# Optimization experiments

Measured on AMD Instinct MI355X. Metric: run time of the kernel, lower is better.

## Reference

```python
import jax, jax.numpy as jnp
import numpy as np

NHEAD = 4
LAYER_TYPES = ["self", "cross", "self", "cross", "semantic_subspace_cross"]


def _ln(x):
    m = jnp.mean(x, axis=-1, keepdims=True)
    v = jnp.var(x, axis=-1, keepdims=True)
    return (x - m) / jnp.sqrt(v + 1e-5)


def _attn(x, source, q_mask, kv_mask, qW, kW, vW, mW, w1, w2):
    # Faithful GeometryAttentionLayer forward (pe=None, sinusoidal branch).
    bs, L, C = x.shape
    dim = C // NHEAD
    qw = (x @ qW).reshape(bs, L, NHEAD, dim)
    kw = (source @ kW).reshape(bs, -1, NHEAD, dim)
    vw = (source @ vW).reshape(bs, -1, NHEAD, dim)
    a = jnp.einsum('nlhd,nshd->nlsh', qw, kw)
    if q_mask is not None:
        bad = q_mask[:, :, None, None] & (~kv_mask)[:, None, :, None]
        a = jnp.where(bad, -jnp.inf, a)
    a = jax.nn.softmax(a / jnp.sqrt(jnp.asarray(dim, x.dtype)), axis=2)
    o = jnp.einsum('nlsh,nshd->nlhd', a, vw).reshape(bs, L, C)
    msg = _ln(o @ mW)
    h = jnp.concatenate([x, msg], axis=-1)
    msg = _ln(jnp.maximum(h @ w1, 0.0) @ w2)
    return x + msg


def setup_inputs() -> dict:
    key = jax.random.key(0)
    ks = jax.random.split(key, 24)
    B, N, C, D2 = 2, 2048, 256, 384
    G, Lp, nL = 16, 512, len(LAYER_TYPES)
    inp = {
        'src_feat': jax.random.normal(ks[0], (B, N, C), jnp.float32),
        'tgt_feat': jax.random.normal(ks[1], (B, N, C), jnp.float32),
        's_pcd': jax.random.normal(ks[2], (B, N, 3), jnp.float32),
        't_pcd': jax.random.normal(ks[3], (B, N, 3), jnp.float32),
        'src_mask': jnp.ones((B, N), bool),
        'tgt_mask': jnp.ones((B, N), bool),
        'src_sub_ind_padded': jax.random.randint(ks[4], (G, Lp), 0, N + 1),
        'tgt_sub_ind_padded': jax.random.randint(ks[5], (G, Lp), 0, N + 1),
        'src_sub_ind_padded_mask': jnp.ones((G, Lp), bool),
        'tgt_sub_ind_padded_mask': jnp.ones((G, Lp), bool),
        'semantic_masks_valid': jnp.ones((G,), bool),
        'src_2dfeat': jax.random.normal(ks[6], (B, N, D2), jnp.float32),
        'tgt_2dfeat': jax.random.normal(ks[7], (B, N, D2), jnp.float32),
        'data': 0,
        'dinoW': jax.random.normal(ks[8], (D2, C), jnp.float32) / np.sqrt(D2),
        'qW': jax.random.normal(ks[9], (nL, C, C), jnp.float32) / np.sqrt(C),
        'kW': jax.random.normal(ks[10], (nL, C, C), jnp.float32) / np.sqrt(C),
        'vW': jax.random.normal(ks[11], (nL, C, C), jnp.float32) / np.sqrt(C),
        'mW': jax.random.normal(ks[12], (nL, C, C), jnp.float32) / np.sqrt(C),
        'w1': jax.random.normal(ks[13], (nL, 2 * C, 2 * C), jnp.float32) / np.sqrt(2 * C),
        'w2': jax.random.normal(ks[14], (nL, 2 * C, C), jnp.float32) / np.sqrt(2 * C),
    }
    return inp


def reference(src_feat, tgt_feat, s_pcd, t_pcd, src_mask, tgt_mask,
              src_sub_ind_padded, tgt_sub_ind_padded,
              src_sub_ind_padded_mask, tgt_sub_ind_padded_mask,
              semantic_masks_valid, src_2dfeat, tgt_2dfeat, data,
              dinoW, qW, kW, vW, mW, w1, w2):
    src2 = src_2dfeat @ dinoW
    tgt2 = tgt_2dfeat @ dinoW
    s_sem = t_sem = None
    for i, name in enumerate(LAYER_TYPES):
        P = (qW[i], kW[i], vW[i], mW[i], w1[i], w2[i])
        if name == 'self':
            src_feat = src_feat + src2
            tgt_feat = tgt_feat + tgt2
            src_feat = _attn(src_feat, src_feat, src_mask, src_mask, *P)
            tgt_feat = _attn(tgt_feat, tgt_feat, tgt_mask, tgt_mask, *P)
        elif name == 'cross':
            src_feat = _attn(src_feat, tgt_feat, src_mask, tgt_mask, *P)
            tgt_feat = _attn(tgt_feat, src_feat, tgt_mask, src_mask, *P)
        else:  # semantic_subspace_cross
            B, N, C = src_feat.shape
            G = src_sub_ind_padded.shape[0]
            mask_num = G // B
            se = jnp.repeat(src_feat[:, None], mask_num, axis=1).reshape(G, N, C)
            te = jnp.repeat(tgt_feat[:, None], mask_num, axis=1).reshape(G, N, C)
            # boolean-select valid semantic groups (all valid in this config,
            # so fixed-size nonzero is exact)
            vidx = jnp.nonzero(semantic_masks_valid, size=G, fill_value=0)[0]
            se, te = se[vidx], te[vidx]
            si, ti = src_sub_ind_padded[vidx], tgt_sub_ind_padded[vidx]
            sm, tm = src_sub_ind_padded_mask[vidx], tgt_sub_ind_padded_mask[vidx]
            # append zero row so pad index N gathers zeros
            se = jnp.concatenate([se, jnp.zeros_like(se[:, :1])], axis=1)
            te = jnp.concatenate([te, jnp.zeros_like(te[:, :1])], axis=1)
            ssub = jnp.take_along_axis(se, si[:, :, None], axis=1)
            tsub = jnp.take_along_axis(te, ti[:, :, None], axis=1)
            s_sem = _attn(ssub, tsub, ~sm, ~tm, *P)
            t_sem = _attn(tsub, ssub, ~tm, ~sm, *P)
    return (src_feat, tgt_feat, s_sem, t_sem)
```

## Files before the change

### kernel.cpp

```cpp
#include <hip/hip_runtime.h>
#include <hip/hip_bf16.h>
#include <cstdint>
#include <cstddef>


typedef __attribute__((ext_vector_type(8))) short bf16x8;
typedef __attribute__((ext_vector_type(4))) float f32x4;

__device__ __forceinline__ float b2f(unsigned short u) {
  union { unsigned int i; float f; } v; v.i = ((unsigned int)u) << 16; return v.f;
}
__device__ __forceinline__ unsigned short f2b(float f) {
  __hip_bfloat16 h = __float2bfloat16(f);
  union { __hip_bfloat16 h; unsigned short u; } v; v.h = h; return v.u;
}
__device__ __forceinline__ unsigned int pk2(float a, float b) {
  return (unsigned int)f2b(a) | ((unsigned int)f2b(b) << 16);
}
__device__ __forceinline__ float fexp2(float x) {
#if __has_builtin(__builtin_amdgcn_exp2f)
  return __builtin_amdgcn_exp2f(x);
#else
  float r; asm("v_exp_f32 %0, %1" : "=v"(r) : "v"(x)); return r;
#endif
}

__global__ __launch_bounds__(256) void k_probe(int* __restrict__ flag,
                                               const unsigned short* __restrict__ w,
                                               int n) {
  __shared__ int ok[256];
  const int t = threadIdx.x;
  int good = 1;
  for (int i = t; i < n; i += 256) {
    float v = fabsf(b2f(w[i]));
    if (!(v < 1e3f)) good = 0;
  }
  ok[t] = good;
  __syncthreads();
  for (int s = 128; s; s >>= 1) {
    if (t < s) ok[t] &= ok[t + s];
    __syncthreads();
  }
  if (t == 0) *flag = ok[0];
}

__global__ __launch_bounds__(256) void k_load2(float* __restrict__ dF,
                                               unsigned short* __restrict__ dB,
                                               const void* __restrict__ src,
                                               int n4, const int* __restrict__ flag) {
  int i = blockIdx.x * 256 + threadIdx.x;
  if (i >= n4) return;
  float4 f;
  if (*flag) {
    ushort4 u = ((const ushort4*)src)[i];
    f.x = b2f(u.x); f.y = b2f(u.y); f.z = b2f(u.z); f.w = b2f(u.w);
  } else {
    f = ((const float4*)src)[i];
  }
  ((float4*)dF)[i] = f;
  ushort4 o; o.x = f2b(f.x); o.y = f2b(f.y); o.z = f2b(f.z); o.w = f2b(f.w);
  ((ushort4*)dB)[i] = o;
}

__global__ __launch_bounds__(256) void k_loadb(unsigned short* __restrict__ dB,
                                               const void* __restrict__ src,
                                               int n4, const int* __restrict__ flag) {
  int i = blockIdx.x * 256 + threadIdx.x;
  if (i >= n4) return;
  if (*flag) {
    ((ushort4*)dB)[i] = ((const ushort4*)src)[i];
    return;
  }
  float4 f = ((const float4*)src)[i];
  ushort4 o; o.x = f2b(f.x); o.y = f2b(f.y); o.z = f2b(f.z); o.w = f2b(f.w);
  ((ushort4*)dB)[i] = o;
}

__global__ __launch_bounds__(256) void k_store(void* __restrict__ out, size_t off,
                                               const float* __restrict__ src,
                                               int n4, const int* __restrict__ flag) {
  int i = blockIdx.x * 256 + threadIdx.x;
  if (i >= n4) return;
  float4 f = ((const float4*)src)[i];
  if (*flag) {
    ushort4 u; u.x = f2b(f.x); u.y = f2b(f.y); u.z = f2b(f.z); u.w = f2b(f.w);
    ((ushort4*)((unsigned short*)out + off))[i] = u;
  } else {
    ((float4*)((float*)out + off))[i] = f;
  }
}

__global__ __launch_bounds__(256) void k_add_dino(float* __restrict__ xF,
                                                  unsigned short* __restrict__ xB,
                                                  const unsigned short* __restrict__ addB,
                                                  int n4) {
  int i = blockIdx.x * 256 + threadIdx.x;
  if (i >= n4) return;
  float4 a = ((const float4*)xF)[i];
  ushort4 u = ((const ushort4*)addB)[i];
  a.x += b2f(u.x); a.y += b2f(u.y); a.z += b2f(u.z); a.w += b2f(u.w);
  ((float4*)xF)[i] = a;
  ushort4 o; o.x = f2b(a.x); o.y = f2b(a.y); o.z = f2b(a.z); o.w = f2b(a.w);
  ((ushort4*)xB)[i] = o;
}

__global__ __launch_bounds__(256) void k_wt(unsigned short* __restrict__ Wt,
                                            const void* __restrict__ W,
                                            int K, int N, int zStride,
                                            const int* __restrict__ flag) {
  __shared__ float tile[32][33];
  const int isbf = *flag;
  const int z = blockIdx.z;
  const unsigned short* Wb = (const unsigned short*)W + (size_t)z * K * N;
  const float* Wf = (const float*)W + (size_t)z * K * N;
  unsigned short* Wo = Wt + (size_t)z * zStride;
  const int KS = K >> 5;
  const int nx = blockIdx.x * 32, ky = blockIdx.y * 32;
  const int tx = threadIdx.x & 31, ty = threadIdx.x >> 5;
#pragma unroll
  for (int i = 0; i < 4; ++i) {
    int k = ky + ty + i * 8;
    float v = isbf ? b2f(Wb[(size_t)k * N + nx + tx]) : Wf[(size_t)k * N + nx + tx];
    tile[ty + i * 8][tx] = v;
  }
  __syncthreads();
  const int kstep = ky >> 5;
  const int lanehi = (tx >> 3) << 4;
  const int e = tx & 7;
#pragma unroll
  for (int i = 0; i < 4; ++i) {
    int nn = ty + i * 8;
    int n_ = nx + nn;
    size_t idx = ((((size_t)(n_ >> 4) * KS + kstep) << 6) + (lanehi + (n_ & 15))) * 8 + e;
    Wo[idx] = f2b(tile[tx][nn]);
  }
}

template<int KTOT>
__global__ __launch_bounds__(256, 4) void k_gmm(unsigned short* __restrict__ Y, int ldy,
                                                const unsigned short* __restrict__ A1, int lda1,
                                                const unsigned short* __restrict__ A2, int lda2,
                                                int K1,
                                                const unsigned short* __restrict__ Wt,
                                                int relu, int rowOff, int rowXor,
                                                int xorColStart, int qkvLog2L) {
  constexpr int KS = KTOT >> 5;
  const int tid = threadIdx.x;
  const int wq = tid >> 6, lane = tid & 63;
  const int l16 = lane & 15, quad = lane >> 4;
  const int gx = gridDim.x;
  const int nwg = gx * gridDim.y;
  const int lid = blockIdx.y * gx + blockIdx.x;
  const int w = (lid & 7) * (nwg >> 3) + (lid >> 3);
  const int n0 = (w % gx) * 64, m0 = (w / gx) * 64;
  const int row = m0 + wq * 16 + l16;
  int arow = rowOff + row;
  if (n0 >= xorColStart) arow ^= rowXor;

  const unsigned short* Wb0 = Wt + ((size_t)(n0 >> 4) * KS << 6) * 8 + (size_t)lane * 8;

  f32x4 acc[4];
#pragma unroll
  for (int i = 0; i < 4; ++i) acc[i] = (f32x4){0.f, 0.f, 0.f, 0.f};

  auto ldA = [&](int k0) -> bf16x8 {
    const unsigned short* ap = (k0 < K1)
        ? (A1 + (size_t)arow * lda1 + k0)
        : (A2 + (size_t)arow * lda2 + (k0 - K1));
    return *(const bf16x8*)(ap + quad * 8);
  };
  auto ldB = [&](int k0, int nb) -> bf16x8 {
    return *(const bf16x8*)(Wb0 + ((size_t)nb * KS + (k0 >> 5)) * 512);
  };

  bf16x8 a0 = ldA(0), a1;
  bf16x8 b0[4], b1[4];
#pragma unroll
  for (int nb = 0; nb < 4; ++nb) b0[nb] = ldB(0, nb);

#pragma unroll
  for (int k0 = 0; k0 < KTOT; k0 += 64) {
    a1 = ldA(k0 + 32);
#pragma unroll
    for (int nb = 0; nb < 4; ++nb) b1[nb] = ldB(k0 + 32, nb);
#pragma unroll
    for (int nb = 0; nb < 4; ++nb)
      acc[nb] = __builtin_amdgcn_mfma_f32_16x16x32_bf16(a0, b0[nb], acc[nb], 0, 0, 0);
    if (k0 + 64 < KTOT) {
      a0 = ldA(k0 + 64);
#pragma unroll
      for (int nb = 0; nb < 4; ++nb) b0[nb] = ldB(k0 + 64, nb);
    }
#pragma unroll
    for (int nb = 0; nb < 4; ++nb)
      acc[nb] = __builtin_amdgcn_mfma_f32_16x16x32_bf16(a1, b1[nb], acc[nb], 0, 0, 0);
  }

  if (qkvLog2L) {
    const int Lm = (1 << qkvLog2L) - 1;
    const int sel = n0 >> 8;
    const int hh = (n0 >> 6) & 3;
    unsigned short* base = Y + (size_t)sel * ((size_t)gridDim.y << 14);
#pragma unroll
    for (int r = 0; r < 4; ++r) {
      const int rr = m0 + wq * 16 + quad * 4 + r;
      const int tok = rr & Lm;
      const int hi = ((rr >> qkvLog2L) << 2) + hh;
      unsigned short* yp = base + ((((size_t)hi << qkvLog2L) + tok) << 6) + l16;
#pragma unroll
      for (int nb = 0; nb < 4; ++nb) yp[nb * 16] = f2b(acc[nb][r]);
    }
  } else {
#pragma unroll
    for (int r = 0; r < 4; ++r) {
      unsigned short* yp = Y + (size_t)(m0 + wq * 16 + quad * 4 + r) * ldy + n0;
#pragma unroll
      for (int nb = 0; nb < 4; ++nb) {
        float v = acc[nb][r];
        if (relu) v = fmaxf(v, 0.f);
        yp[nb * 16 + l16] = f2b(v);
      }
    }
  }
}

__device__ __forceinline__ void row_stats(float4 v, float& mean, float& inv) {
  float s  = v.x + v.y + v.z + v.w;
  float s2 = fmaf(v.x, v.x, fmaf(v.y, v.y, fmaf(v.z, v.z, v.w * v.w)));
#pragma unroll
  for (int off = 32; off >= 1; off >>= 1) {
    s  += __shfl_xor(s,  off, 64);
    s2 += __shfl_xor(s2, off, 64);
  }
  mean = s * (1.f / 256.f);
  float var = s2 * (1.f / 256.f) - mean * mean;
  inv = rsqrtf(var + 1e-5f);
}

template<int KTOT>
__global__ __launch_bounds__(256, 4) void k_gmm_ln(unsigned short* __restrict__ Yb,
                                                   float* __restrict__ xF,
                                                   void* __restrict__ outp, size_t outOff,
                                                   const unsigned short* __restrict__ xBres,
                                                   const unsigned short* __restrict__ A1,
                                                   int lda1,
                                                   const unsigned short* __restrict__ Wt,
                                                   int mode, const int* __restrict__ flag) {
  constexpr int KS = KTOT >> 5;
  __shared__ float Ot[16][260];
  const int tid = threadIdx.x;
  const int wq = tid >> 6, lane = tid & 63;
  const int l16 = lane & 15, quad = lane >> 4;
  const int nwg = gridDim.x;
  const int lid = blockIdx.x;
  const int w = (lid & 7) * (nwg >> 3) + (lid >> 3);
  const int R0 = w * 16;

  const unsigned short* Wb0 = Wt + ((size_t)(wq * 4) * KS << 6) * 8 + (size_t)lane * 8;
  const unsigned short* Ap = A1 + (size_t)(R0 + l16) * lda1;

  f32x4 acc[4];
#pragma unroll
  for (int i = 0; i < 4; ++i) acc[i] = (f32x4){0.f, 0.f, 0.f, 0.f};

  auto ldA = [&](int k0) -> bf16x8 { return *(const bf16x8*)(Ap + k0 + quad * 8); };
  auto ldB = [&](int k0, int nb) -> bf16x8 {
    return *(const bf16x8*)(Wb0 + ((size_t)nb * KS + (k0 >> 5)) * 512);
  };

  bf16x8 a0 = ldA(0), a1;
  bf16x8 b0[4], b1[4];
#pragma unroll
  for (int nb = 0; nb < 4; ++nb) b0[nb] = ldB(0, nb);

#pragma unroll
  for (int k0 = 0; k0 < KTOT; k0 += 64) {
    a1 = ldA(k0 + 32);
#pragma unroll
    for (int nb = 0; nb < 4; ++nb) b1[nb] = ldB(k0 + 32, nb);
#pragma unroll
    for (int nb = 0; nb < 4; ++nb)
      acc[nb] = __builtin_amdgcn_mfma_f32_16x16x32_bf16(a0, b0[nb], acc[nb], 0, 0, 0);
    if (k0 + 64 < KTOT) {
      a0 = ldA(k0 + 64);
#pragma unroll
      for (int nb = 0; nb < 4; ++nb) b0[nb] = ldB(k0 + 64, nb);
    }
#pragma unroll
    for (int nb = 0; nb < 4; ++nb)
      acc[nb] = __builtin_amdgcn_mfma_f32_16x16x32_bf16(a1, b1[nb], acc[nb], 0, 0, 0);
  }

#pragma unroll
  for (int nb = 0; nb < 4; ++nb)
#pragma unroll
    for (int r = 0; r < 4; ++r)
      Ot[quad * 4 + r][wq * 64 + nb * 16 + l16] = acc[nb][r];
  __syncthreads();

#pragma unroll
  for (int rr = 0; rr < 4; ++rr) {
    const int row = rr * 4 + wq;
    float4 v = *(const float4*)&Ot[row][lane * 4];
    float mean, inv; row_stats(v, mean, inv);
    float4 nv;
    nv.x = (v.x - mean) * inv; nv.y = (v.y - mean) * inv;
    nv.z = (v.z - mean) * inv; nv.w = (v.w - mean) * inv;
    const size_t gr = (size_t)(R0 + row) * 256 + lane * 4;
    if (mode == 0) {
      ushort4 u; u.x = f2b(nv.x); u.y = f2b(nv.y); u.z = f2b(nv.z); u.w = f2b(nv.w);
      *(ushort4*)(Yb + gr) = u;
    } else if (mode == 1) {
      float4 xv = *(const float4*)(xF + gr);
      float4 rs;
      rs.x = xv.x + nv.x; rs.y = xv.y + nv.y; rs.z = xv.z + nv.z; rs.w = xv.w + nv.w;
      *(float4*)(xF + gr) = rs;
      ushort4 u; u.x = f2b(rs.x); u.y = f2b(rs.y); u.z = f2b(rs.z); u.w = f2b(rs.w);
      *(ushort4*)(Yb + gr) = u;
    } else {
      ushort4 xu = *(const ushort4*)(xBres + gr);
      float4 rs;
      rs.x = b2f(xu.x) + nv.x; rs.y = b2f(xu.y) + nv.y;
      rs.z = b2f(xu.z) + nv.z; rs.w = b2f(xu.w) + nv.w;
      if (*flag) {
        ushort4 u; u.x = f2b(rs.x); u.y = f2b(rs.y); u.z = f2b(rs.z); u.w = f2b(rs.w);
        *(ushort4*)((unsigned short*)outp + outOff + gr) = u;
      } else {
        *(float4*)((float*)outp + outOff + gr) = rs;
      }
    }
  }
}

__global__ __launch_bounds__(512, 4) void k_attn_p(float* __restrict__ pO,
                                                   float* __restrict__ pML,
                                                   const unsigned short* __restrict__ QKV,
                                                   unsigned long long kOff,
                                                   int L, int S, int chunk) {
  __shared__ __align__(16) char smem[34816];
  unsigned short* Kl = (unsigned short*)smem;
  unsigned short (*Vt)[64][72] = (unsigned short (*)[64][72])(smem + 16384);
  const int tid = threadIdx.x;
  const int wq = tid >> 6, lane = tid & 63;
  const int l16 = lane & 15, quad = lane >> 4;
  const int q0 = blockIdx.x * 256;
  const int nh = blockIdx.y, NHt = gridDim.y;
  const int s0 = blockIdx.z * chunk;
  const float S2 = 0.18033688f;

  const unsigned short* Qh = QKV + (size_t)nh * L * 64;
  const unsigned short* Kh = QKV + kOff + (size_t)nh * S * 64;
  const unsigned short* Vh = QKV + 2 * kOff + (size_t)nh * S * 64;

  bf16x8 qa[2][2];
#pragma unroll
  for (int qb = 0; qb < 2; ++qb) {
    const unsigned short* qp = Qh + (size_t)(q0 + (qb * 8 + wq) * 16 + l16) * 64;
    qa[qb][0] = *(const bf16x8*)(qp + quad * 8);
    qa[qb][1] = *(const bf16x8*)(qp + 32 + quad * 8);
  }

  const short ONE = (short)0x3F80;
  const bf16x8 onesv = (bf16x8){ONE, ONE, ONE, ONE, ONE, ONE, ONE, ONE};

  f32x4 acc[2][4];
  f32x4 lacc[2];
#pragma unroll
  for (int qb = 0; qb < 2; ++qb) {
#pragma unroll
    for (int i = 0; i < 4; ++i) acc[qb][i] = (f32x4){0.f, 0.f, 0.f, 0.f};
    lacc[qb] = (f32x4){0.f, 0.f, 0.f, 0.f};
  }
  float m_[2] = {-1e30f, -1e30f};

  const int skey = tid >> 3;
  const int sdh0 = (tid & 7) * 8;
  const int kidx = (((skey >> 4) * 2 + (sdh0 >> 5)) * 64 +
                    (((sdh0 >> 3) & 3) * 16) + ((skey & 15) ^ (tid & 7))) * 8;
  const int krd0 = lane ^ quad;
  const int krd1 = lane ^ (4 | quad);
  const int vdh0 = wq * 8;
  const int pc = ((lane >> 5) << 5) + (((lane >> 2) & 3) << 3)
               + (((lane >> 4) & 1) << 2) + (lane & 3);

  uint4 kv = *(const uint4*)(Kh + (size_t)(s0 + skey) * 64 + sdh0);
  uint4 va = *(const uint4*)(Vh + (size_t)(s0 + lane) * 64 + vdh0);
  *(uint4*)&Kl[kidx] = kv;
  {
    const unsigned short* pv = (const unsigned short*)&va;
#pragma unroll
    for (int i = 0; i < 8; ++i) Vt[0][vdh0 + i][pc] = pv[i];
  }
  if (chunk > 64) {
    kv = *(const uint4*)(Kh + (size_t)(s0 + 64 + skey) * 64 + sdh0);
    va = *(const uint4*)(Vh + (size_t)(s0 + 64 + lane) * 64 + vdh0);
  }
  __syncthreads();

  int cur = 0;
  for (int t = 0; t < chunk; t += 64) {
    f32x4 sc[2][4];
    const unsigned short* Klc = Kl + cur * 4096;
    __builtin_amdgcn_s_setprio(1);
#pragma unroll
    for (int kb = 0; kb < 4; ++kb) {
      bf16x8 kf0 = *(const bf16x8*)&Klc[((kb * 2 + 0) * 64 + krd0) * 8];
      bf16x8 kf1 = *(const bf16x8*)&Klc[((kb * 2 + 1) * 64 + krd1) * 8];
#pragma unroll
      for (int qb = 0; qb < 2; ++qb) {
        f32x4 z = (f32x4){0.f, 0.f, 0.f, 0.f};
        z = __builtin_amdgcn_mfma_f32_16x16x32_bf16(kf0, qa[qb][0], z, 0, 0, 0);
        z = __builtin_amdgcn_mfma_f32_16x16x32_bf16(kf1, qa[qb][1], z, 0, 0, 0);
        sc[qb][kb] = z;
      }
    }
    __builtin_amdgcn_s_setprio(0);
    if (t + 64 < chunk) {
      *(uint4*)&Kl[(cur ^ 1) * 4096 + kidx] = kv;
      const unsigned short* pv = (const unsigned short*)&va;
#pragma unroll
      for (int i = 0; i < 8; ++i) Vt[cur ^ 1][vdh0 + i][pc] = pv[i];
    }
    if (t + 128 < chunk) {
      kv = *(const uint4*)(Kh + (size_t)(s0 + t + 128 + skey) * 64 + sdh0);
      va = *(const uint4*)(Vh + (size_t)(s0 + t + 128 + lane) * 64 + vdh0);
    }
    union { bf16x8 v; unsigned int w[4]; } ps0[2], ps1[2];
#pragma unroll
    for (int qb = 0; qb < 2; ++qb) {
      f32x4 mv01, mv;
#pragma unroll
      for (int r = 0; r < 4; ++r) mv01[r] = fmaxf(sc[qb][0][r], sc[qb][1][r]);
#pragma unroll
      for (int r = 0; r < 4; ++r) mv[r] = fmaxf(mv01[r], fmaxf(sc[qb][2][r], sc[qb][3][r]));
      float mx = fmaxf(fmaxf(mv[0], mv[1]), fmaxf(mv[2], mv[3])) * S2;
      mx = fmaxf(mx, __shfl_xor(mx, 16));
      mx = fmaxf(mx, __shfl_xor(mx, 32));
      float mn;
      if (__all(mx <= m_[qb] + 8.f)) {
        mn = m_[qb];
      } else {
        mn = fmaxf(m_[qb], mx);
        float alpha = fexp2(m_[qb] - mn);
        m_[qb] = mn;
#pragma unroll
        for (int r = 0; r < 4; ++r) lacc[qb][r] *= alpha;
#pragma unroll
        for (int nb = 0; nb < 4; ++nb)
#pragma unroll
          for (int r = 0; r < 4; ++r) acc[qb][nb][r] *= alpha;
      }
#pragma unroll
      for (int kb = 0; kb < 4; ++kb)
#pragma unroll
        for (int r = 0; r < 4; ++r)
          sc[qb][kb][r] = fexp2(fmaf(sc[qb][kb][r], S2, -mn));
      ps0[qb].w[0] = pk2(sc[qb][0][0], sc[qb][0][1]);
      ps0[qb].w[1] = pk2(sc[qb][0][2], sc[qb][0][3]);
      ps0[qb].w[2] = pk2(sc[qb][1][0], sc[qb][1][1]);
      ps0[qb].w[3] = pk2(sc[qb][1][2], sc[qb][1][3]);
      ps1[qb].w[0] = pk2(sc[qb][2][0], sc[qb][2][1]);
      ps1[qb].w[1] = pk2(sc[qb][2][2], sc[qb][2][3]);
      ps1[qb].w[2] = pk2(sc[qb][3][0], sc[qb][3][1]);
      ps1[qb].w[3] = pk2(sc[qb][3][2], sc[qb][3][3]);
    }
    __builtin_amdgcn_s_setprio(1);
#pragma unroll
    for (int db = 0; db < 4; ++db) {
      bf16x8 vb0 = *(const bf16x8*)&Vt[cur][db * 16 + l16][quad * 8];
      bf16x8 vb1 = *(const bf16x8*)&Vt[cur][db * 16 + l16][32 + quad * 8];
#pragma unroll
      for (int qb = 0; qb < 2; ++qb) {
        acc[qb][db] = __builtin_amdgcn_mfma_f32_16x16x32_bf16(vb0, ps0[qb].v, acc[qb][db], 0, 0, 0);
        acc[qb][db] = __builtin_amdgcn_mfma_f32_16x16x32_bf16(vb1, ps1[qb].v, acc[qb][db], 0, 0, 0);
      }
    }
#pragma unroll
    for (int qb = 0; qb < 2; ++qb) {
      lacc[qb] = __builtin_amdgcn_mfma_f32_16x16x32_bf16(onesv, ps0[qb].v, lacc[qb], 0, 0, 0);
      lacc[qb] = __builtin_amdgcn_mfma_f32_16x16x32_bf16(onesv, ps1[qb].v, lacc[qb], 0, 0, 0);
    }
    __builtin_amdgcn_s_setprio(0);
    __syncthreads();
    cur ^= 1;
  }

  float* Ot = (float*)smem;
#pragma unroll
  for (int qb = 0; qb < 2; ++qb) {
#pragma unroll
    for (int pass = 0; pass < 2; ++pass) {
      __syncthreads();
      if ((wq >> 2) == pass) {
#pragma unroll
        for (int db = 0; db < 4; ++db)
          *(f32x4*)&Ot[(size_t)((wq & 3) * 16 + l16) * 68 + db * 16 + quad * 4] = acc[qb][db];
      }
      __syncthreads();
      if ((wq >> 2) == pass) {
#pragma unroll
        for (int i = 0; i < 16; ++i) {
          const int row = q0 + (qb * 8 + wq) * 16 + i;
          pO[((size_t)(blockIdx.z * NHt + nh) * L + row) * 64 + lane] =
              Ot[(size_t)((wq & 3) * 16 + i) * 68 + lane];
        }
      }
    }
  }
  if (quad == 0) {
#pragma unroll
    for (int qb = 0; qb < 2; ++qb) {
      float* pml = pML + ((size_t)(blockIdx.z * NHt + nh) * L +
                          q0 + (qb * 8 + wq) * 16 + l16) * 2;
      pml[0] = m_[qb]; pml[1] = lacc[qb][0];
    }
  }
}

__global__ __launch_bounds__(256) void k_attn_c(unsigned short* __restrict__ O,
                                                const float* __restrict__ pO,
                                                const float* __restrict__ pML,
                                                int L, int split) {
  const int tid = threadIdx.x;
  const int q = blockIdx.x * 64 + (tid >> 2);
  const int part = tid & 3;
  const int nh = blockIdx.y, NHt = gridDim.y;
  const int n = nh >> 2, h = nh & 3;

  float M = -1e30f;
  for (int sp = 0; sp < split; ++sp)
    M = fmaxf(M, pML[(((size_t)sp * NHt + nh) * L + q) * 2]);

  float4 acc[4];
#pragma unroll
  for (int i = 0; i < 4; ++i) { acc[i].x = 0.f; acc[i].y = 0.f; acc[i].z = 0.f; acc[i].w = 0.f; }
  float lsum = 0.f;
  for (int sp = 0; sp < split; ++sp) {
    const float* pml = pML + (((size_t)sp * NHt + nh) * L + q) * 2;
    float e = fexp2(pml[0] - M);
    lsum = fmaf(pml[1], e, lsum);
    const float4* po = (const float4*)(pO + (((size_t)sp * NHt + nh) * L + q) * 64 + part * 16);
#pragma unroll
    for (int i = 0; i < 4; ++i) {
      float4 v = po[i];
      acc[i].x = fmaf(v.x, e, acc[i].x);
      acc[i].y = fmaf(v.y, e, acc[i].y);
      acc[i].z = fmaf(v.z, e, acc[i].z);
      acc[i].w = fmaf(v.w, e, acc[i].w);
    }
  }
  float inv = 1.0f / lsum;
  unsigned short* op = O + ((size_t)(n * L + q)) * 256 + h * 64 + part * 16;
#pragma unroll
  for (int i = 0; i < 4; ++i) {
    ushort4 u;
    u.x = f2b(acc[i].x * inv); u.y = f2b(acc[i].y * inv);
    u.z = f2b(acc[i].z * inv); u.w = f2b(acc[i].w * inv);
    ((ushort4*)op)[i] = u;
  }
}

__global__ __launch_bounds__(64) void k_gather2(unsigned short* __restrict__ dst,
                                                const float* __restrict__ sF,
                                                const int* __restrict__ sIdx,
                                                const int* __restrict__ tIdx) {
  const int row = blockIdx.x;
  const int half = row >> 13;
  const int r = row & 8191;
  const int g = r >> 9;
  const int b = g >> 3;
  const int id = half ? tIdx[r] : sIdx[r];
  float4 v = {0.f, 0.f, 0.f, 0.f};
  if ((unsigned)id < 2048u) {
    const float* base = sF + (size_t)(half * 2 + b) * 524288;
    v = ((const float4*)(base + (size_t)id * 256))[threadIdx.x];
  }
  ushort4 u; u.x = f2b(v.x); u.y = f2b(v.y); u.z = f2b(v.z); u.w = f2b(v.w);
  ((ushort4*)(dst + (size_t)row * 256))[threadIdx.x] = u;
}

extern "C" void kernel_launch(void* const* d_in, const int* in_sizes, int n_in,
                              void* d_out, int out_size, void* d_ws, size_t ws_size,
                              hipStream_t stream) {
  const void* src_feat = d_in[0];
  const void* tgt_feat = d_in[1];
  const int* s_sub = (const int*)d_in[6];
  const int* t_sub = (const int*)d_in[7];
  const void* src2d = d_in[11];
  const void* tgt2d = d_in[12];
  const void* dinoW = d_in[14];
  const void* qW = d_in[15];
  const void* kW = d_in[16];
  const void* vW = d_in[17];
  const void* mW = d_in[18];
  const void* w1 = d_in[19];
  const void* w2 = d_in[20];

  const int BIG = 1 << 30;
  char* p = (char*)d_ws;
  int* dflag = (int*)p;                       p += 256;
  float* sF = (float*)p;                      p += 4194304;
  float* tF = (float*)p;                      p += 4194304;
  unsigned short* sB    = (unsigned short*)p; p += 2097152;
  unsigned short* tB    = (unsigned short*)p; p += 2097152;
  unsigned short* s2B   = (unsigned short*)p; p += 2097152;
  unsigned short* t2B   = (unsigned short*)p; p += 2097152;
  unsigned short* d2B   = (unsigned short*)p; p += 3145728;
  unsigned short* sSubB = (unsigned short*)p; p += 4194304;
  unsigned short* tSubB = (unsigned short*)p; p += 4194304;
  unsigned short* qkvB  = (unsigned short*)p;
  unsigned short* msgB  = (unsigned short*)(p + 8388608);
  unsigned short* oB    = (unsigned short*)(p + 16777216);
  p += 25165824;
  unsigned short* hB    = (unsigned short*)p;
  p += 25165824;
  unsigned short* WtD   = (unsigned short*)p; p += 196608;
  unsigned short* WtQKV = (unsigned short*)p; p += 1966080;
  unsigned short* WtM   = (unsigned short*)p; p += 655360;
  unsigned short* WtW1  = (unsigned short*)p; p += 2621440;
  unsigned short* WtW2  = (unsigned short*)p; p += 1310720;
  float* pO  = (float*)p;                     p += 33554432;
  float* pML = (float*)p;                     p += 2097152;

  k_probe<<<1, 256, 0, stream>>>(dflag, (const unsigned short*)qW, 4096);

  k_wt<<<dim3(8, 12, 1), 256, 0, stream>>>(WtD, dinoW, 384, 256, 0, dflag);
  k_wt<<<dim3(8, 8, 5), 256, 0, stream>>>(WtQKV,          qW, 256, 256, 196608, dflag);
  k_wt<<<dim3(8, 8, 5), 256, 0, stream>>>(WtQKV + 65536,  kW, 256, 256, 196608, dflag);
  k_wt<<<dim3(8, 8, 5), 256, 0, stream>>>(WtQKV + 131072, vW, 256, 256, 196608, dflag);
  k_wt<<<dim3(8, 8, 5), 256, 0, stream>>>(WtM, mW, 256, 256, 65536, dflag);
  k_wt<<<dim3(16, 16, 5), 256, 0, stream>>>(WtW1, w1, 512, 512, 262144, dflag);
  k_wt<<<dim3(8, 16, 5), 256, 0, stream>>>(WtW2, w2, 512, 256, 131072, dflag);

  auto attnB = [&](int l, const unsigned short* Abase, int rowOff, int rowXor,
                   int M, int L, int S, int split, int NHt,
                   float* xF, unsigned short* xB, size_t outOff) {
    const int lg = (L == 2048) ? 11 : 9;
    k_gmm<256><<<dim3(12, M / 64), 256, 0, stream>>>(
        qkvB, 768, Abase, 256, Abase, 256, 256,
        WtQKV + (size_t)l * 196608, 0, rowOff, rowXor, 256, lg);
    const int chunk = S / split;
    k_attn_p<<<dim3(L / 256, NHt, split), 512, 0, stream>>>(
        pO, pML, qkvB, (unsigned long long)M * 256, L, S, chunk);
    k_attn_c<<<dim3(L / 64, NHt), 256, 0, stream>>>(oB, pO, pML, L, split);
    k_gmm_ln<256><<<M / 16, 256, 0, stream>>>(
        msgB, nullptr, nullptr, 0, nullptr, oB, 256,
        WtM + (size_t)l * 65536, 0, dflag);
    k_gmm<512><<<dim3(8, M / 64), 256, 0, stream>>>(
        hB, 512, xB, 256, msgB, 256, 256, WtW1 + (size_t)l * 262144, 1, 0, 0, BIG, 0);
    if (xF) k_gmm_ln<512><<<M / 16, 256, 0, stream>>>(
        xB, xF, nullptr, 0, nullptr, hB, 512, WtW2 + (size_t)l * 131072, 1, dflag);
    else    k_gmm_ln<512><<<M / 16, 256, 0, stream>>>(
        nullptr, nullptr, d_out, outOff, xB, hB, 512, WtW2 + (size_t)l * 131072, 2, dflag);
  };

  k_load2<<<1024, 256, 0, stream>>>(sF, sB, src_feat, 262144, dflag);
  k_load2<<<1024, 256, 0, stream>>>(tF, tB, tgt_feat, 262144, dflag);
  k_loadb<<<1536, 256, 0, stream>>>(d2B, src2d, 393216, dflag);
  k_gmm<384><<<dim3(4, 64), 256, 0, stream>>>(s2B, 256, d2B, 384, d2B, 384, 384,
                                              WtD, 0, 0, 0, BIG, 0);
  k_loadb<<<1536, 256, 0, stream>>>(d2B, tgt2d, 393216, dflag);
  k_gmm<384><<<dim3(4, 64), 256, 0, stream>>>(t2B, 256, d2B, 384, d2B, 384, 384,
                                              WtD, 0, 0, 0, BIG, 0);

  k_add_dino<<<2048, 256, 0, stream>>>(sF, sB, s2B, 524288);
  attnB(0, sB, 0, 0, 8192, 2048, 2048, 4, 16, sF, sB, 0);
  attnB(1, sB, 0,    4096, 4096, 2048, 2048, 8, 8, sF, sB, 0);
  attnB(1, sB, 4096, 4096, 4096, 2048, 2048, 8, 8, tF, tB, 0);
  k_add_dino<<<2048, 256, 0, stream>>>(sF, sB, s2B, 524288);
  attnB(2, sB, 0, 0, 8192, 2048, 2048, 4, 16, sF, sB, 0);
  attnB(3, sB, 0,    4096, 4096, 2048, 2048, 8, 8, sF, sB, 0);
  attnB(3, sB, 4096, 4096, 4096, 2048, 2048, 8, 8, tF, tB, 0);
  k_gather2<<<16384, 64, 0, stream>>>(sSubB, sF, s_sub, t_sub);
  attnB(4, sSubB, 0, 8192, 16384, 512, 512, 2, 128, nullptr, sSubB, 2097152);

  k_store<<<2048, 256, 0, stream>>>(d_out, 0, sF, 524288, dflag);
}
```

Before: 782.1 us.

## Fuse split-attention combine into merge projection with LayerNorm

Adds a kernel that merges the split-KV partial attention outputs (max/sum rescale) directly into shared memory as bf16 and then runs the merge-projection MFMA GEMM and LayerNorm, replacing the separate combine kernel and the standalone projection launch. This removes one launch per attention block and the write and re-read of the intermediate O buffer. The gather kernel is also regrouped to handle four rows per 256-thread block. The fused kernel does the combine with only 16 rows per block, so the reads of partial outputs may be less efficient.

```diff
diff --git a/kernel.cpp b/kernel.cpp
--- a/kernel.cpp
+++ b/kernel.cpp
@@ -307,10 +307,7 @@
     nv.x = (v.x - mean) * inv; nv.y = (v.y - mean) * inv;
     nv.z = (v.z - mean) * inv; nv.w = (v.w - mean) * inv;
     const size_t gr = (size_t)(R0 + row) * 256 + lane * 4;
-    if (mode == 0) {
-      ushort4 u; u.x = f2b(nv.x); u.y = f2b(nv.y); u.z = f2b(nv.z); u.w = f2b(nv.w);
-      *(ushort4*)(Yb + gr) = u;
-    } else if (mode == 1) {
+    if (mode == 1) {
       float4 xv = *(const float4*)(xF + gr);
       float4 rs;
       rs.x = xv.x + nv.x; rs.y = xv.y + nv.y; rs.z = xv.z + nv.z; rs.w = xv.w + nv.w;
@@ -332,6 +329,123 @@
   }
 }
 
+__global__ __launch_bounds__(256, 4) void k_mprojc(unsigned short* __restrict__ msgB,
+                                                   const float* __restrict__ pO,
+                                                   const float* __restrict__ pML,
+                                                   int lgL, int split, int NHt,
+                                                   const unsigned short* __restrict__ Wt) {
+  constexpr int KS = 8;
+  __shared__ __align__(16) char smem[16640];
+  unsigned short* At = (unsigned short*)smem;
+  float (*Ot)[260] = (float (*)[260])smem;
+  const int tid = threadIdx.x;
+  const int wq = tid >> 6, lane = tid & 63;
+  const int l16 = lane & 15, quad = lane >> 4;
+  const int nwg = gridDim.x;
+  const int lid = blockIdx.x;
+  const int w = (lid & 7) * (nwg >> 3) + (lid >> 3);
+  const int R0 = w * 16;
+  const int L = 1 << lgL, Lm = L - 1;
+
+  {
+    const int i = tid >> 4;
+    const int c = tid & 15;
+    const int gr = R0 + i;
+    const int n = gr >> lgL;
+    const int tok = gr & Lm;
+    const int nh = n * 4 + (c >> 2);
+    float M = -1e30f;
+    for (int sp = 0; sp < split; ++sp)
+      M = fmaxf(M, pML[(((size_t)sp * NHt + nh) * L + tok) * 2]);
+    float4 a0 = {0,0,0,0}, a1 = {0,0,0,0}, a2 = {0,0,0,0}, a3 = {0,0,0,0};
+    float lsum = 0.f;
+    for (int sp = 0; sp < split; ++sp) {
+      const float* pml = pML + (((size_t)sp * NHt + nh) * L + tok) * 2;
+      float e = fexp2(pml[0] - M);
+      lsum = fmaf(pml[1], e, lsum);
+      const float4* po = (const float4*)(pO + (((size_t)sp * NHt + nh) * L + tok) * 64
+                                         + (c & 3) * 16);
+      float4 v0 = po[0], v1 = po[1], v2 = po[2], v3 = po[3];
+      a0.x = fmaf(v0.x, e, a0.x); a0.y = fmaf(v0.y, e, a0.y);
+      a0.z = fmaf(v0.z, e, a0.z); a0.w = fmaf(v0.w, e, a0.w);
+      a1.x = fmaf(v1.x, e, a1.x); a1.y = fmaf(v1.y, e, a1.y);
+      a1.z = fmaf(v1.z, e, a1.z); a1.w = fmaf(v1.w, e, a1.w);
+      a2.x = fmaf(v2.x, e, a2.x); a2.y = fmaf(v2.y, e, a2.y);
+      a2.z = fmaf(v2.z, e, a2.z); a2.w = fmaf(v2.w, e, a2.w);
+      a3.x = fmaf(v3.x, e, a3.x); a3.y = fmaf(v3.y, e, a3.y);
+      a3.z = fmaf(v3.z, e, a3.z); a3.w = fmaf(v3.w, e, a3.w);
+    }
+    float inv = 1.0f / lsum;
+    union { unsigned short us[8]; uint4 v; } p0, p1;
+    p0.us[0] = f2b(a0.x * inv); p0.us[1] = f2b(a0.y * inv);
+    p0.us[2] = f2b(a0.z * inv); p0.us[3] = f2b(a0.w * inv);
+    p0.us[4] = f2b(a1.x * inv); p0.us[5] = f2b(a1.y * inv);
+    p0.us[6] = f2b(a1.z * inv); p0.us[7] = f2b(a1.w * inv);
+    p1.us[0] = f2b(a2.x * inv); p1.us[1] = f2b(a2.y * inv);
+    p1.us[2] = f2b(a2.z * inv); p1.us[3] = f2b(a2.w * inv);
+    p1.us[4] = f2b(a3.x * inv); p1.us[5] = f2b(a3.y * inv);
+    p1.us[6] = f2b(a3.z * inv); p1.us[7] = f2b(a3.w * inv);
+    const int u0 = (2 * c) ^ (i & 7);
+    const int u1 = (2 * c + 1) ^ (i & 7);
+    *(uint4*)&At[((i << 5) + u0) * 8] = p0.v;
+    *(uint4*)&At[((i << 5) + u1) * 8] = p1.v;
+  }
+  __syncthreads();
+
+  const unsigned short* Wb0 = Wt + ((size_t)(wq * 4) * KS << 6) * 8 + (size_t)lane * 8;
+  f32x4 acc[4];
+#pragma unroll
+  for (int i = 0; i < 4; ++i) acc[i] = (f32x4){0.f, 0.f, 0.f, 0.f};
+
+  auto ldA = [&](int k0) -> bf16x8 {
+    const int u = (k0 >> 3) + quad;
+    return *(const bf16x8*)&At[((l16 << 5) + (u ^ (l16 & 7))) * 8];
+  };
+  auto ldB = [&](int k0, int nb) -> bf16x8 {
+    return *(const bf16x8*)(Wb0 + ((size_t)nb * KS + (k0 >> 5)) * 512);
+  };
+
+  bf16x8 b0[4], b1[4];
+#pragma unroll
+  for (int nb = 0; nb < 4; ++nb) b0[nb] = ldB(0, nb);
+#pragma unroll
+  for (int k0 = 0; k0 < 256; k0 += 64) {
+#pragma unroll
+    for (int nb = 0; nb < 4; ++nb) b1[nb] = ldB(k0 + 32, nb);
+    bf16x8 a0 = ldA(k0);
+#pragma unroll
+    for (int nb = 0; nb < 4; ++nb)
+      acc[nb] = __builtin_amdgcn_mfma_f32_16x16x32_bf16(a0, b0[nb], acc[nb], 0, 0, 0);
+    if (k0 + 64 < 256) {
+#pragma unroll
+      for (int nb = 0; nb < 4; ++nb) b0[nb] = ldB(k0 + 64, nb);
+    }
+    bf16x8 a1 = ldA(k0 + 32);
+#pragma unroll
+    for (int nb = 0; nb < 4; ++nb)
+      acc[nb] = __builtin_amdgcn_mfma_f32_16x16x32_bf16(a1, b1[nb], acc[nb], 0, 0, 0);
+  }
+  __syncthreads();
+
+#pragma unroll
+  for (int nb = 0; nb < 4; ++nb)
+#pragma unroll
+    for (int r = 0; r < 4; ++r)
+      Ot[quad * 4 + r][wq * 64 + nb * 16 + l16] = acc[nb][r];
+  __syncthreads();
+
+#pragma unroll
+  for (int rr = 0; rr < 4; ++rr) {
+    const int row = rr * 4 + wq;
+    float4 v = *(const float4*)&Ot[row][lane * 4];
+    float mean, inv; row_stats(v, mean, inv);
+    ushort4 u;
+    u.x = f2b((v.x - mean) * inv); u.y = f2b((v.y - mean) * inv);
+    u.z = f2b((v.z - mean) * inv); u.w = f2b((v.w - mean) * inv);
+    *(ushort4*)(msgB + (size_t)(R0 + row) * 256 + lane * 4) = u;
+  }
+}
+
 __global__ __launch_bounds__(512, 4) void k_attn_p(float* __restrict__ pO,
                                                    float* __restrict__ pML,
                                                    const unsigned short* __restrict__ QKV,
@@ -517,54 +631,12 @@
   }
 }
 
-__global__ __launch_bounds__(256) void k_attn_c(unsigned short* __restrict__ O,
-                                                const float* __restrict__ pO,
-                                                const float* __restrict__ pML,
-                                                int L, int split) {
-  const int tid = threadIdx.x;
-  const int q = blockIdx.x * 64 + (tid >> 2);
-  const int part = tid & 3;
-  const int nh = blockIdx.y, NHt = gridDim.y;
-  const int n = nh >> 2, h = nh & 3;
-
-  float M = -1e30f;
-  for (int sp = 0; sp < split; ++sp)
-    M = fmaxf(M, pML[(((size_t)sp * NHt + nh) * L + q) * 2]);
-
-  float4 acc[4];
-#pragma unroll
-  for (int i = 0; i < 4; ++i) { acc[i].x = 0.f; acc[i].y = 0.f; acc[i].z = 0.f; acc[i].w = 0.f; }
-  float lsum = 0.f;
-  for (int sp = 0; sp < split; ++sp) {
-    const float* pml = pML + (((size_t)sp * NHt + nh) * L + q) * 2;
-    float e = fexp2(pml[0] - M);
-    lsum = fmaf(pml[1], e, lsum);
-    const float4* po = (const float4*)(pO + (((size_t)sp * NHt + nh) * L + q) * 64 + part * 16);
-#pragma unroll
-    for (int i = 0; i < 4; ++i) {
-      float4 v = po[i];
-      acc[i].x = fmaf(v.x, e, acc[i].x);
-      acc[i].y = fmaf(v.y, e, acc[i].y);
-      acc[i].z = fmaf(v.z, e, acc[i].z);
-      acc[i].w = fmaf(v.w, e, acc[i].w);
-    }
-  }
-  float inv = 1.0f / lsum;
-  unsigned short* op = O + ((size_t)(n * L + q)) * 256 + h * 64 + part * 16;
-#pragma unroll
-  for (int i = 0; i < 4; ++i) {
-    ushort4 u;
-    u.x = f2b(acc[i].x * inv); u.y = f2b(acc[i].y * inv);
-    u.z = f2b(acc[i].z * inv); u.w = f2b(acc[i].w * inv);
-    ((ushort4*)op)[i] = u;
-  }
-}
-
-__global__ __launch_bounds__(64) void k_gather2(unsigned short* __restrict__ dst,
-                                                const float* __restrict__ sF,
-                                                const int* __restrict__ sIdx,
-                                                const int* __restrict__ tIdx) {
-  const int row = blockIdx.x;
+__global__ __launch_bounds__(256) void k_gather2(unsigned short* __restrict__ dst,
+                                                 const float* __restrict__ sF,
+                                                 const int* __restrict__ sIdx,
+                                                 const int* __restrict__ tIdx) {
+  const int row = blockIdx.x * 4 + (threadIdx.x >> 6);
+  const int t = threadIdx.x & 63;
   const int half = row >> 13;
   const int r = row & 8191;
   const int g = r >> 9;
@@ -573,10 +645,10 @@
   float4 v = {0.f, 0.f, 0.f, 0.f};
   if ((unsigned)id < 2048u) {
     const float* base = sF + (size_t)(half * 2 + b) * 524288;
-    v = ((const float4*)(base + (size_t)id * 256))[threadIdx.x];
+    v = ((const float4*)(base + (size_t)id * 256))[t];
   }
   ushort4 u; u.x = f2b(v.x); u.y = f2b(v.y); u.z = f2b(v.z); u.w = f2b(v.w);
-  ((ushort4*)(dst + (size_t)row * 256))[threadIdx.x] = u;
+  ((ushort4*)(dst + (size_t)row * 256))[t] = u;
 }
 
 extern "C" void kernel_launch(void* const* d_in, const int* in_sizes, int n_in,
@@ -610,7 +682,6 @@
   unsigned short* tSubB = (unsigned short*)p; p += 4194304;
   unsigned short* qkvB  = (unsigned short*)p;
   unsigned short* msgB  = (unsigned short*)(p + 8388608);
-  unsigned short* oB    = (unsigned short*)(p + 16777216);
   p += 25165824;
   unsigned short* hB    = (unsigned short*)p;
   p += 25165824;
@@ -642,10 +713,8 @@
     const int chunk = S / split;
     k_attn_p<<<dim3(L / 256, NHt, split), 512, 0, stream>>>(
         pO, pML, qkvB, (unsigned long long)M * 256, L, S, chunk);
-    k_attn_c<<<dim3(L / 64, NHt), 256, 0, stream>>>(oB, pO, pML, L, split);
-    k_gmm_ln<256><<<M / 16, 256, 0, stream>>>(
-        msgB, nullptr, nullptr, 0, nullptr, oB, 256,
-        WtM + (size_t)l * 65536, 0, dflag);
+    k_mprojc<<<M / 16, 256, 0, stream>>>(msgB, pO, pML, lg, split, NHt,
+                                         WtM + (size_t)l * 65536);
     k_gmm<512><<<dim3(8, M / 64), 256, 0, stream>>>(
         hB, 512, xB, 256, msgB, 256, 256, WtW1 + (size_t)l * 262144, 1, 0, 0, BIG, 0);
     if (xF) k_gmm_ln<512><<<M / 16, 256, 0, stream>>>(
@@ -671,7 +740,7 @@
   attnB(2, sB, 0, 0, 8192, 2048, 2048, 4, 16, sF, sB, 0);
   attnB(3, sB, 0,    4096, 4096, 2048, 2048, 8, 8, sF, sB, 0);
   attnB(3, sB, 4096, 4096, 4096, 2048, 2048, 8, 8, tF, tB, 0);
-  k_gather2<<<16384, 64, 0, stream>>>(sSubB, sF, s_sub, t_sub);
+  k_gather2<<<4096, 256, 0, stream>>>(sSubB, sF, s_sub, t_sub);
   attnB(4, sSubB, 0, 8192, 16384, 512, 512, 2, 128, nullptr, sSubB, 2097152);
 
   k_store<<<2048, 256, 0, stream>>>(d_out, 0, sF, 524288, dflag);
```

New measurement: 738.1 us (median of 2 runs). 1.06x faster.
